# Performance work log

Hardware: AMD Instinct MI355X
Metric: run time of the kernel (lower is better)

Reference implementation:

```python
import jax, jax.numpy as jnp
import numpy as np

N, D, H = 2048, 1024, 16
DH = D // H
SCALE = 1.0 / DH ** 0.5


def setup_inputs() -> dict:
    key = jax.random.key(0)
    k0, k1, k2 = jax.random.split(key, 3)
    lim_qkv = 1.0 / np.sqrt(D)
    lim_proj = 1.0 / np.sqrt(D)
    return {
        "x": jax.random.normal(k0, (N, D), dtype=jnp.float32),
        "w_qkv": jax.random.uniform(k1, (3 * D, D), jnp.float32, -lim_qkv, lim_qkv),
        "b_qkv": jnp.zeros((3 * D,), jnp.float32),
        "w_proj": jax.random.uniform(k2, (D, D), jnp.float32, -lim_proj, lim_proj),
        "b_proj": jnp.zeros((D,), jnp.float32),
    }


def reference(x, w_qkv, b_qkv, w_proj, b_proj) -> jnp.ndarray:
    # qkv linear: (N, D) -> (N, 3D)
    qkv = x @ w_qkv.T + b_qkv
    q, k, v = jnp.split(qkv, 3, axis=-1)
    # (N, D) -> (H, N, Dh)
    def _heads(a):
        return a.reshape(N, H, DH).transpose(1, 0, 2)
    q, k, v = map(_heads, (q, k, v))
    # full NxN scores per head (faithful to original einsum+softmax)
    attn = jax.nn.softmax(jnp.einsum('hnd,hmd->hnm', q * SCALE, k), axis=-1)
    out = jnp.einsum('hnm,hmd->hnd', attn, v)          # (H, N, Dh)
    out = out.transpose(1, 0, 2).reshape(N, D)
    return out @ w_proj.T + b_proj
```

## Files before the change

kernel.cpp:

```cpp
#include <hip/hip_runtime.h>
#include <hip/hip_bf16.h>
#include <cstdint>

typedef unsigned short u16;
typedef __attribute__((ext_vector_type(8)))  short bf16x8;
typedef __attribute__((ext_vector_type(4)))  float f32x4;
typedef __attribute__((ext_vector_type(16))) float f32x16;
typedef __attribute__((ext_vector_type(2)))  unsigned int uint2v;

#define N_TOK   2048
#define DMODEL  1024
#define NHEAD   16
#define DHEAD   64
#define QKV_N   3072
#define QK_LD   2048
#define NSPLIT  4
#define KV_PER  (N_TOK / NSPLIT)
#define C1_LOG2 0.1803368801111244f
#define M0_BASE 4.0f

__device__ __forceinline__ u16 f2b(float f) {
  uint32_t u = __float_as_uint(f);
  u += 0x7FFFu + ((u >> 16) & 1u);
  return (u16)(u >> 16);
}
__device__ __forceinline__ float b2f(u16 b) {
  return __uint_as_float(((uint32_t)b) << 16);
}
__device__ __forceinline__ float fexp2(float x) { return __builtin_amdgcn_exp2f(x); }

__device__ __forceinline__ uint32_t cvtpk(float lo, float hi) {
  uint32_t r;
  asm("v_cvt_pk_bf16_f32 %0, %1, %2" : "=v"(r) : "v"(lo), "v"(hi));
  return r;
}

__device__ __forceinline__ float xsum32(float x) {
  uint2v d = __builtin_amdgcn_permlane32_swap(__float_as_uint(x), __float_as_uint(x), false, false);
  return __uint_as_float(d.x) + __uint_as_float(d.y);
}

__device__ __forceinline__ void gload_lds16(const void* g, void* l) {
  __builtin_amdgcn_global_load_lds(
      (const __attribute__((address_space(1))) void*)g,
      (__attribute__((address_space(3))) void*)l,
      16, 0, 0);
}

__global__ __launch_bounds__(256)
void cvt_all(const float* __restrict__ x, const float* __restrict__ wq,
             const float* __restrict__ wp,
             u16* __restrict__ xb, u16* __restrict__ wqb, u16* __restrict__ wpb) {
  const int i = blockIdx.x * 256 + threadIdx.x;
  const int NX = (N_TOK * DMODEL) / 4;
  const int NQ = (3 * DMODEL * DMODEL) / 4;
  const float4* src; u16* dst; int j;
  if (i < NX)            { src = (const float4*)x;  dst = xb;  j = i; }
  else if (i < NX + NQ)  { src = (const float4*)wq; dst = wqb; j = i - NX; }
  else                   { src = (const float4*)wp; dst = wpb; j = i - NX - NQ; }
  const float4 v = src[j];
  ushort4 pk;
  pk.x = f2b(v.x); pk.y = f2b(v.y); pk.z = f2b(v.z); pk.w = f2b(v.w);
  ((ushort4*)dst)[j] = pk;
}

template<bool OUT_F32, bool FUSE_VT, int MI, int NI>
__global__ __launch_bounds__(256, 2)
void gemm_nt(const u16* __restrict__ A, const u16* __restrict__ B,
             const float* __restrict__ bias, void* __restrict__ Cv,
             u16* __restrict__ vtg, int ldc, int K) {
  __shared__ alignas(16) u16 As[2][MI * 32 * 64];
  __shared__ alignas(16) u16 Bs[2][NI * 32 * 64];
  const int tid = threadIdx.x;
  const int w = tid >> 6, l = tid & 63;
  const int lo = l & 15, hi = l >> 4;
  const int wr = w >> 1, wc = w & 1;
  const int bm = blockIdx.y * (MI * 32), bn = blockIdx.x * (NI * 32);
  f32x4 acc[MI][NI] = {};
  const int NK = K >> 6;

  auto stage = [&](int kb, int bufi) {
#pragma unroll
    for (int i = 0; i < MI; ++i) {
      const int c = w * (MI * 64) + i * 64 + l;
      const int r = c >> 3, gs = (c ^ r) & 7;
      gload_lds16(A + (size_t)(bm + r) * K + kb + gs * 8, (char*)As[bufi] + (size_t)c * 16);
    }
#pragma unroll
    for (int i = 0; i < NI; ++i) {
      const int c = w * (NI * 64) + i * 64 + l;
      const int r = c >> 3, gs = (c ^ r) & 7;
      gload_lds16(B + (size_t)(bn + r) * K + kb + gs * 8, (char*)Bs[bufi] + (size_t)c * 16);
    }
  };

  stage(0, 0);
  int buf = 0;
  for (int t = 0; t < NK; ++t) {
    if (t + 1 < NK) {
      stage((t + 1) * 64, buf ^ 1);
      if constexpr (MI + NI == 7)      asm volatile("s_waitcnt vmcnt(7)" ::: "memory");
      else if constexpr (MI + NI == 6) asm volatile("s_waitcnt vmcnt(6)" ::: "memory");
      else if constexpr (MI + NI == 4) asm volatile("s_waitcnt vmcnt(4)" ::: "memory");
      else                             asm volatile("s_waitcnt vmcnt(8)" ::: "memory");
    } else {
      asm volatile("s_waitcnt vmcnt(0)" ::: "memory");
    }
    __builtin_amdgcn_s_barrier();

    bf16x8 af[MI][2], bfr[NI][2];
#pragma unroll
    for (int mi = 0; mi < MI; ++mi)
#pragma unroll
      for (int ks = 0; ks < 2; ++ks) {
        const int ra = wr * (MI * 16) + mi * 16 + lo;
        af[mi][ks] = *(const bf16x8*)((const char*)As[buf] + ra * 128 +
                                      (((ks * 4 + hi) ^ (ra & 7)) << 4));
      }
#pragma unroll
    for (int ni = 0; ni < NI; ++ni)
#pragma unroll
      for (int ks = 0; ks < 2; ++ks) {
        const int rb = wc * (NI * 16) + ni * 16 + lo;
        bfr[ni][ks] = *(const bf16x8*)((const char*)Bs[buf] + rb * 128 +
                                       (((ks * 4 + hi) ^ (rb & 7)) << 4));
      }
#pragma unroll
    for (int mi = 0; mi < MI; ++mi)
#pragma unroll
      for (int ni = 0; ni < NI; ++ni)
#pragma unroll
        for (int ks = 0; ks < 2; ++ks)
          acc[mi][ni] = __builtin_amdgcn_mfma_f32_16x16x32_bf16(af[mi][ks], bfr[ni][ks], acc[mi][ni], 0, 0, 0);

    __builtin_amdgcn_s_barrier();
    buf ^= 1;
  }

#pragma unroll
  for (int mi = 0; mi < MI; ++mi)
#pragma unroll
    for (int ni = 0; ni < NI; ++ni) {
      const int col = bn + wc * (NI * 16) + ni * 16 + lo;
      const float bv = bias[col];
      if constexpr (FUSE_VT) {
        if (col >= 2 * DMODEL) {
          const int row0 = bm + wr * (MI * 16) + mi * 16 + hi * 4;
          ushort4 pk;
          pk.x = f2b(acc[mi][ni][0] + bv);
          pk.y = f2b(acc[mi][ni][1] + bv);
          pk.z = f2b(acc[mi][ni][2] + bv);
          pk.w = f2b(acc[mi][ni][3] + bv);
          *(ushort4*)(vtg + (size_t)(col - 2 * DMODEL) * N_TOK + row0) = pk;
        } else {
          const float sc = (col < DMODEL) ? C1_LOG2 : 1.0f;
#pragma unroll
          for (int j = 0; j < 4; ++j) {
            const int row = bm + wr * (MI * 16) + mi * 16 + hi * 4 + j;
            ((u16*)Cv)[(size_t)row * QK_LD + col] = f2b((acc[mi][ni][j] + bv) * sc);
          }
        }
      } else {
#pragma unroll
        for (int j = 0; j < 4; ++j) {
          const int row = bm + wr * (MI * 16) + mi * 16 + hi * 4 + j;
          const float v = acc[mi][ni][j] + bv;
          if constexpr (OUT_F32) ((float*)Cv)[(size_t)row * ldc + col] = v;
          else                   ((u16*)Cv)[(size_t)row * ldc + col] = f2b(v);
        }
      }
    }
}

#define FRAG(BASE, ROW, SLOT) \
  (*(const bf16x8*)((const char*)(BASE) + (ROW) * 128 + ((((SLOT) ^ ((ROW) & 7))) << 4)))

__global__ __launch_bounds__(256, 4)
void attn3(const u16* __restrict__ qkb, const u16* __restrict__ vtg,
           u16* __restrict__ PO, float* __restrict__ lbuf) {
  __shared__ alignas(16) u16 Kt[2][64 * 64];
  __shared__ alignas(16) u16 Vt[2][64 * 64];
  const int tid = threadIdx.x;
  const int w = tid >> 6, l = tid & 63;
  const int lo = l & 31, hi = l >> 5;

  int bid = (int)blockIdx.x;
  bid = (bid & 7) * 128 + (bid >> 3);
  const int h  = bid >> 6;
  const int qb = (bid >> 2) & 15;
  const int z  = bid & 3;
  const int q0 = qb * 128 + w * 32;
  const int kv0 = z * KV_PER;

  bf16x8 qf[4];
  const u16* qsrc = qkb + (size_t)(q0 + lo) * QK_LD + h * 64 + hi * 8;
#pragma unroll
  for (int ds = 0; ds < 4; ++ds) qf[ds] = *(const bf16x8*)(qsrc + ds * 16);

  f32x16 o0 = {}, o1 = {};
  float lsum = 0.f;

#define STAGE(KB, B) do {                                                       \
    _Pragma("unroll")                                                           \
    for (int i_ = 0; i_ < 2; ++i_) {                                            \
      const int c_ = w * 128 + i_ * 64 + l;                                     \
      const int r_ = c_ >> 3;                                                   \
      const int gs_ = (c_ ^ r_) & 7;                                            \
      gload_lds16(qkb + (size_t)((KB) + r_) * QK_LD + DMODEL + h * 64 + gs_ * 8,\
                  (char*)Kt[B] + (size_t)(w * 128 + i_ * 64) * 16);             \
      gload_lds16(vtg + (size_t)(h * 64 + r_) * N_TOK + (KB) + gs_ * 8,         \
                  (char*)Vt[B] + (size_t)(w * 128 + i_ * 64) * 16);             \
    }                                                                           \
  } while (0)

  STAGE(kv0, 0);
  int buf = 0;
  for (int t = 0; t < KV_PER / 64; ++t) {
    if (t + 1 < KV_PER / 64) {
      STAGE(kv0 + (t + 1) * 64, buf ^ 1);
      asm volatile("s_waitcnt vmcnt(4)" ::: "memory");
    } else {
      asm volatile("s_waitcnt vmcnt(0)" ::: "memory");
    }
    __builtin_amdgcn_s_barrier();

    const u16* Kb = Kt[buf];
    const u16* Vb = Vt[buf];

    f32x16 s0 = {}, s1 = {};
    __builtin_amdgcn_s_setprio(1);
#pragma unroll
    for (int ds = 0; ds < 4; ++ds) {
      bf16x8 k0 = FRAG(Kb, lo, ds * 2 + hi);
      bf16x8 k1 = FRAG(Kb, 32 + lo, ds * 2 + hi);
      s0 = __builtin_amdgcn_mfma_f32_32x32x16_bf16(k0, qf[ds], s0, 0, 0, 0);
      s1 = __builtin_amdgcn_mfma_f32_32x32x16_bf16(k1, qf[ds], s1, 0, 0, 0);
    }
    __builtin_amdgcn_s_setprio(0);

    float tsum = 0.f;
    bf16x8 pfr[4];
#pragma unroll
    for (int ks = 0; ks < 4; ++ks) {
      float q[8];
#pragma unroll
      for (int j = 0; j < 8; ++j) {
        const int idx = (ks & 1) * 8 + j;
        q[j] = fexp2(((ks < 2) ? s0[idx] : s1[idx]) - M0_BASE);
      }
      tsum += ((q[0] + q[1]) + (q[2] + q[3])) + ((q[4] + q[5]) + (q[6] + q[7]));
      uint32_t a1 = cvtpk(q[0], q[1]);
      uint32_t a2 = cvtpk(q[2], q[3]);
      uint32_t b1 = cvtpk(q[4], q[5]);
      uint32_t b2 = cvtpk(q[6], q[7]);
      uint2v r1 = __builtin_amdgcn_permlane32_swap(a1, b1, false, false);
      uint2v r2 = __builtin_amdgcn_permlane32_swap(a2, b2, false, false);
      union { uint32_t u[4]; bf16x8 h; } cv;
      cv.u[0] = r1.x; cv.u[1] = r2.x; cv.u[2] = r1.y; cv.u[3] = r2.y;
      pfr[ks] = cv.h;
    }
    lsum += tsum;

    __builtin_amdgcn_s_setprio(1);
#pragma unroll
    for (int ks = 0; ks < 4; ++ks) {
      bf16x8 v0 = FRAG(Vb, lo, ks * 2 + hi);
      bf16x8 v1 = FRAG(Vb, 32 + lo, ks * 2 + hi);
      o0 = __builtin_amdgcn_mfma_f32_32x32x16_bf16(v0, pfr[ks], o0, 0, 0, 0);
      o1 = __builtin_amdgcn_mfma_f32_32x32x16_bf16(v1, pfr[ks], o1, 0, 0, 0);
    }
    __builtin_amdgcn_s_setprio(0);

    __builtin_amdgcn_s_barrier();
    buf ^= 1;
  }
#undef STAGE

  lsum = xsum32(lsum);

  u16* Ow = ((u16*)Kt) + w * 2048;
  const float inv = 1.0f / lsum;
#pragma unroll
  for (int r = 0; r < 16; ++r) {
    const int crow = (r & 3) + 8 * (r >> 2) + 4 * hi;
    const int c0 = crow, c1 = 32 + crow;
    Ow[lo * 64 + (((c0 >> 3) ^ (lo & 7)) << 3) + (c0 & 7)] = f2b(o0[r] * inv);
    Ow[lo * 64 + (((c1 >> 3) ^ (lo & 7)) << 3) + (c1 & 7)] = f2b(o1[r] * inv);
  }
  if (hi == 0)
    lbuf[((size_t)z * NHEAD + h) * N_TOK + q0 + lo] = lsum;
  asm volatile("s_waitcnt lgkmcnt(0)" ::: "memory");
  __builtin_amdgcn_sched_barrier(0);
  u16* pobase = PO + (((size_t)z * NHEAD + h) * N_TOK + q0) * DHEAD;
#pragma unroll
  for (int i = 0; i < 4; ++i) {
    const int c = i * 64 + l;
    const int rr = c >> 3, sl = c & 7;
    bf16x8 v = *(const bf16x8*)(Ow + rr * 64 + sl * 8);
    const int cs = sl ^ (rr & 7);
    *(bf16x8*)(pobase + (size_t)rr * DHEAD + cs * 8) = v;
  }
}

__global__ __launch_bounds__(256)
void combine(const u16* __restrict__ PO, const float* __restrict__ lbuf,
             u16* __restrict__ attb) {
  const int idx = blockIdx.x * 256 + threadIdx.x;
  const int row = idx >> 3;
  const int c8  = (idx & 7) * 8;
  const int h = row >> 11;
  const int q = row & (N_TOK - 1);

  float wsum = 0.f, acc8[8] = {};
#pragma unroll
  for (int zz = 0; zz < NSPLIT; ++zz) {
    const float wz = lbuf[((size_t)zz * NHEAD + h) * N_TOK + q];
    wsum += wz;
    bf16x8 po = *(const bf16x8*)(PO + (((size_t)zz * NHEAD + h) * N_TOK + q) * DHEAD + c8);
#pragma unroll
    for (int j = 0; j < 8; ++j) acc8[j] += wz * b2f((u16)po[j]);
  }
  const float invw = 1.0f / wsum;
  union { u16 s[8]; bf16x8 h8; } ov;
#pragma unroll
  for (int j = 0; j < 8; ++j) ov.s[j] = f2b(acc8[j] * invw);
  *(bf16x8*)(attb + (size_t)q * DMODEL + h * 64 + c8) = ov.h8;
}

extern "C" void kernel_launch(void* const* d_in, const int* in_sizes, int n_in,
                              void* d_out, int out_size, void* d_ws, size_t ws_size,
                              hipStream_t stream) {
  const float* x      = (const float*)d_in[0];
  const float* w_qkv  = (const float*)d_in[1];
  const float* b_qkv  = (const float*)d_in[2];
  const float* w_proj = (const float*)d_in[3];
  const float* b_proj = (const float*)d_in[4];
  float* out = (float*)d_out;

  char* ws = (char*)d_ws;
  u16*    xb     = (u16*)(ws + (0u  << 20));
  u16*    wqkvb  = (u16*)(ws + (8u  << 20));
  u16*    wprojb = (u16*)(ws + (16u << 20));
  u16*    qkb    = (u16*)(ws + (24u << 20));
  u16*    vtg    = (u16*)(ws + (40u << 20));
  u16*    PO     = (u16*)(ws + (48u << 20));
  float*  lbuf   = (float*)(ws + (64u << 20));
  u16*    attb   = (u16*)(ws + (66u << 20));
  if (ws_size < (80u << 20)) return;

  cvt_all<<<6144, 256, 0, stream>>>(x, w_qkv, w_proj, xb, wqkvb, wprojb);

  gemm_nt<false, true, 4, 3><<<dim3(QKV_N / 96, N_TOK / 128), 256, 0, stream>>>(
      xb, wqkvb, b_qkv, (void*)qkb, vtg, QK_LD, DMODEL);

  attn3<<<16 * NHEAD * NSPLIT, 256, 0, stream>>>(qkb, vtg, PO, lbuf);

  combine<<<(N_TOK * NHEAD * 8) / 256, 256, 0, stream>>>(PO, lbuf, attb);

  gemm_nt<true, false, 2, 2><<<dim3(DMODEL / 64, N_TOK / 64), 256, 0, stream>>>(
      attb, wprojb, b_proj, (void*)out, nullptr, DMODEL, DMODEL);
}
```

Before: 75.95 us.

## Process 64 query rows per wave in attention to reuse K/V tiles

Each attention wave now handles two 32-row query fragments instead of one, so every K and V LDS fragment feeds twice as many MFMAs, and the grid is halved to 512 blocks. Launch bounds drop to 2 blocks per SM to leave room for the doubled accumulators and Q fragments. The output projection GEMM also switches to a 128-row tile. The aim is fewer LDS reads and global K/V loads per unit of work, at the cost of higher register pressure, lower occupancy and fewer blocks to fill the CUs.

```diff
diff --git a/kernel.cpp b/kernel.cpp
--- a/kernel.cpp
+++ b/kernel.cpp
@@ -175,30 +175,57 @@
 #define FRAG(BASE, ROW, SLOT) \
   (*(const bf16x8*)((const char*)(BASE) + (ROW) * 128 + ((((SLOT) ^ ((ROW) & 7))) << 4)))
 
-__global__ __launch_bounds__(256, 4)
+#define SOFTPACK(SA, SB, PFR, LS) do {                                          \
+    float tsum_ = 0.f;                                                          \
+    _Pragma("unroll")                                                           \
+    for (int ks = 0; ks < 4; ++ks) {                                            \
+      float q_[8];                                                              \
+      _Pragma("unroll")                                                         \
+      for (int j = 0; j < 8; ++j) {                                             \
+        const int idx = (ks & 1) * 8 + j;                                       \
+        q_[j] = fexp2(((ks < 2) ? (SA)[idx] : (SB)[idx]) - M0_BASE);            \
+      }                                                                         \
+      tsum_ += ((q_[0] + q_[1]) + (q_[2] + q_[3])) + ((q_[4] + q_[5]) + (q_[6] + q_[7])); \
+      uint32_t a1 = cvtpk(q_[0], q_[1]);                                        \
+      uint32_t a2 = cvtpk(q_[2], q_[3]);                                        \
+      uint32_t b1 = cvtpk(q_[4], q_[5]);                                        \
+      uint32_t b2 = cvtpk(q_[6], q_[7]);                                        \
+      uint2v r1 = __builtin_amdgcn_permlane32_swap(a1, b1, false, false);       \
+      uint2v r2 = __builtin_amdgcn_permlane32_swap(a2, b2, false, false);       \
+      union { uint32_t u[4]; bf16x8 h; } cv_;                                   \
+      cv_.u[0] = r1.x; cv_.u[1] = r2.x; cv_.u[2] = r1.y; cv_.u[3] = r2.y;       \
+      (PFR)[ks] = cv_.h;                                                        \
+    }                                                                           \
+    (LS) += tsum_;                                                              \
+  } while (0)
+
+__global__ __launch_bounds__(256, 2)
 void attn3(const u16* __restrict__ qkb, const u16* __restrict__ vtg,
            u16* __restrict__ PO, float* __restrict__ lbuf) {
-  __shared__ alignas(16) u16 Kt[2][64 * 64];
-  __shared__ alignas(16) u16 Vt[2][64 * 64];
+  __shared__ alignas(16) u16 SMEM[4][64 * 64];
   const int tid = threadIdx.x;
   const int w = tid >> 6, l = tid & 63;
   const int lo = l & 31, hi = l >> 5;
 
   int bid = (int)blockIdx.x;
-  bid = (bid & 7) * 128 + (bid >> 3);
-  const int h  = bid >> 6;
-  const int qb = (bid >> 2) & 15;
+  bid = (bid & 7) * 64 + (bid >> 3);
+  const int h  = bid >> 5;
+  const int qb = (bid >> 2) & 7;
   const int z  = bid & 3;
-  const int q0 = qb * 128 + w * 32;
+  const int q0w = qb * 256 + w * 64;
   const int kv0 = z * KV_PER;
 
-  bf16x8 qf[4];
-  const u16* qsrc = qkb + (size_t)(q0 + lo) * QK_LD + h * 64 + hi * 8;
-#pragma unroll
-  for (int ds = 0; ds < 4; ++ds) qf[ds] = *(const bf16x8*)(qsrc + ds * 16);
-
-  f32x16 o0 = {}, o1 = {};
-  float lsum = 0.f;
+  bf16x8 qf0[4], qf1[4];
+  {
+    const u16* qs0 = qkb + (size_t)(q0w + lo) * QK_LD + h * 64 + hi * 8;
+    const u16* qs1 = qkb + (size_t)(q0w + 32 + lo) * QK_LD + h * 64 + hi * 8;
+#pragma unroll
+    for (int ds = 0; ds < 4; ++ds) { qf0[ds] = *(const bf16x8*)(qs0 + ds * 16);
+                                     qf1[ds] = *(const bf16x8*)(qs1 + ds * 16); }
+  }
+
+  f32x16 o0 = {}, o1 = {}, o2 = {}, o3 = {};
+  float lsum0 = 0.f, lsum1 = 0.f;
 
 #define STAGE(KB, B) do {                                                       \
     _Pragma("unroll")                                                           \
@@ -207,9 +234,9 @@
       const int r_ = c_ >> 3;                                                   \
       const int gs_ = (c_ ^ r_) & 7;                                            \
       gload_lds16(qkb + (size_t)((KB) + r_) * QK_LD + DMODEL + h * 64 + gs_ * 8,\
-                  (char*)Kt[B] + (size_t)(w * 128 + i_ * 64) * 16);             \
+                  (char*)SMEM[B] + (size_t)(w * 128 + i_ * 64) * 16);           \
       gload_lds16(vtg + (size_t)(h * 64 + r_) * N_TOK + (KB) + gs_ * 8,         \
-                  (char*)Vt[B] + (size_t)(w * 128 + i_ * 64) * 16);             \
+                  (char*)SMEM[2 + (B)] + (size_t)(w * 128 + i_ * 64) * 16);     \
     }                                                                           \
   } while (0)
 
@@ -224,50 +251,35 @@
     }
     __builtin_amdgcn_s_barrier();
 
-    const u16* Kb = Kt[buf];
-    const u16* Vb = Vt[buf];
-
-    f32x16 s0 = {}, s1 = {};
+    const u16* Kb = SMEM[buf];
+    const u16* Vb = SMEM[2 + buf];
+
+    f32x16 s0 = {}, s1 = {}, s2 = {}, s3 = {};
     __builtin_amdgcn_s_setprio(1);
 #pragma unroll
     for (int ds = 0; ds < 4; ++ds) {
       bf16x8 k0 = FRAG(Kb, lo, ds * 2 + hi);
       bf16x8 k1 = FRAG(Kb, 32 + lo, ds * 2 + hi);
-      s0 = __builtin_amdgcn_mfma_f32_32x32x16_bf16(k0, qf[ds], s0, 0, 0, 0);
-      s1 = __builtin_amdgcn_mfma_f32_32x32x16_bf16(k1, qf[ds], s1, 0, 0, 0);
+      s0 = __builtin_amdgcn_mfma_f32_32x32x16_bf16(k0, qf0[ds], s0, 0, 0, 0);
+      s1 = __builtin_amdgcn_mfma_f32_32x32x16_bf16(k1, qf0[ds], s1, 0, 0, 0);
+      s2 = __builtin_amdgcn_mfma_f32_32x32x16_bf16(k0, qf1[ds], s2, 0, 0, 0);
+      s3 = __builtin_amdgcn_mfma_f32_32x32x16_bf16(k1, qf1[ds], s3, 0, 0, 0);
     }
     __builtin_amdgcn_s_setprio(0);
 
-    float tsum = 0.f;
-    bf16x8 pfr[4];
-#pragma unroll
-    for (int ks = 0; ks < 4; ++ks) {
-      float q[8];
-#pragma unroll
-      for (int j = 0; j < 8; ++j) {
-        const int idx = (ks & 1) * 8 + j;
-        q[j] = fexp2(((ks < 2) ? s0[idx] : s1[idx]) - M0_BASE);
-      }
-      tsum += ((q[0] + q[1]) + (q[2] + q[3])) + ((q[4] + q[5]) + (q[6] + q[7]));
-      uint32_t a1 = cvtpk(q[0], q[1]);
-      uint32_t a2 = cvtpk(q[2], q[3]);
-      uint32_t b1 = cvtpk(q[4], q[5]);
-      uint32_t b2 = cvtpk(q[6], q[7]);
-      uint2v r1 = __builtin_amdgcn_permlane32_swap(a1, b1, false, false);
-      uint2v r2 = __builtin_amdgcn_permlane32_swap(a2, b2, false, false);
-      union { uint32_t u[4]; bf16x8 h; } cv;
-      cv.u[0] = r1.x; cv.u[1] = r2.x; cv.u[2] = r1.y; cv.u[3] = r2.y;
-      pfr[ks] = cv.h;
-    }
-    lsum += tsum;
+    bf16x8 pfr0[4], pfr1[4];
+    SOFTPACK(s0, s1, pfr0, lsum0);
+    SOFTPACK(s2, s3, pfr1, lsum1);
 
     __builtin_amdgcn_s_setprio(1);
 #pragma unroll
     for (int ks = 0; ks < 4; ++ks) {
       bf16x8 v0 = FRAG(Vb, lo, ks * 2 + hi);
       bf16x8 v1 = FRAG(Vb, 32 + lo, ks * 2 + hi);
-      o0 = __builtin_amdgcn_mfma_f32_32x32x16_bf16(v0, pfr[ks], o0, 0, 0, 0);
-      o1 = __builtin_amdgcn_mfma_f32_32x32x16_bf16(v1, pfr[ks], o1, 0, 0, 0);
+      o0 = __builtin_amdgcn_mfma_f32_32x32x16_bf16(v0, pfr0[ks], o0, 0, 0, 0);
+      o1 = __builtin_amdgcn_mfma_f32_32x32x16_bf16(v1, pfr0[ks], o1, 0, 0, 0);
+      o2 = __builtin_amdgcn_mfma_f32_32x32x16_bf16(v0, pfr1[ks], o2, 0, 0, 0);
+      o3 = __builtin_amdgcn_mfma_f32_32x32x16_bf16(v1, pfr1[ks], o3, 0, 0, 0);
     }
     __builtin_amdgcn_s_setprio(0);
 
@@ -276,24 +288,31 @@
   }
 #undef STAGE
 
-  lsum = xsum32(lsum);
-
-  u16* Ow = ((u16*)Kt) + w * 2048;
-  const float inv = 1.0f / lsum;
+  lsum0 = xsum32(lsum0);
+  lsum1 = xsum32(lsum1);
+
+  u16* Ow = ((u16*)SMEM) + w * 4096;
+  const float inv0 = 1.0f / lsum0;
+  const float inv1 = 1.0f / lsum1;
 #pragma unroll
   for (int r = 0; r < 16; ++r) {
     const int crow = (r & 3) + 8 * (r >> 2) + 4 * hi;
     const int c0 = crow, c1 = 32 + crow;
-    Ow[lo * 64 + (((c0 >> 3) ^ (lo & 7)) << 3) + (c0 & 7)] = f2b(o0[r] * inv);
-    Ow[lo * 64 + (((c1 >> 3) ^ (lo & 7)) << 3) + (c1 & 7)] = f2b(o1[r] * inv);
-  }
-  if (hi == 0)
-    lbuf[((size_t)z * NHEAD + h) * N_TOK + q0 + lo] = lsum;
+    const int s0i = ((c0 >> 3) ^ (lo & 7)) << 3, s1i = ((c1 >> 3) ^ (lo & 7)) << 3;
+    Ow[lo * 64 + s0i + (c0 & 7)] = f2b(o0[r] * inv0);
+    Ow[lo * 64 + s1i + (c1 & 7)] = f2b(o1[r] * inv0);
+    Ow[(32 + lo) * 64 + s0i + (c0 & 7)] = f2b(o2[r] * inv1);
+    Ow[(32 + lo) * 64 + s1i + (c1 & 7)] = f2b(o3[r] * inv1);
+  }
+  if (hi == 0) {
+    lbuf[((size_t)z * NHEAD + h) * N_TOK + q0w + lo] = lsum0;
+    lbuf[((size_t)z * NHEAD + h) * N_TOK + q0w + 32 + lo] = lsum1;
+  }
   asm volatile("s_waitcnt lgkmcnt(0)" ::: "memory");
   __builtin_amdgcn_sched_barrier(0);
-  u16* pobase = PO + (((size_t)z * NHEAD + h) * N_TOK + q0) * DHEAD;
-#pragma unroll
-  for (int i = 0; i < 4; ++i) {
+  u16* pobase = PO + (((size_t)z * NHEAD + h) * N_TOK + q0w) * DHEAD;
+#pragma unroll
+  for (int i = 0; i < 8; ++i) {
     const int c = i * 64 + l;
     const int rr = c >> 3, sl = c & 7;
     bf16x8 v = *(const bf16x8*)(Ow + rr * 64 + sl * 8);
@@ -353,10 +372,10 @@
   gemm_nt<false, true, 4, 3><<<dim3(QKV_N / 96, N_TOK / 128), 256, 0, stream>>>(
       xb, wqkvb, b_qkv, (void*)qkb, vtg, QK_LD, DMODEL);
 
-  attn3<<<16 * NHEAD * NSPLIT, 256, 0, stream>>>(qkb, vtg, PO, lbuf);
+  attn3<<<8 * NHEAD * NSPLIT, 256, 0, stream>>>(qkb, vtg, PO, lbuf);
 
   combine<<<(N_TOK * NHEAD * 8) / 256, 256, 0, stream>>>(PO, lbuf, attb);
 
-  gemm_nt<true, false, 2, 2><<<dim3(DMODEL / 64, N_TOK / 64), 256, 0, stream>>>(
+  gemm_nt<true, false, 4, 2><<<dim3(DMODEL / 64, N_TOK / 128), 256, 0, stream>>>(
       attb, wprojb, b_proj, (void*)out, nullptr, DMODEL, DMODEL);
 }
```

New measurement: 75.67 us. Within noise of the previous version (-0.4%).
